# Kernel optimization log

Hardware: AMD Instinct MI355X
Metric: run time of the kernel (lower is better)

Reference implementation:

```python
import jax, jax.numpy as jnp
import numpy as np

BLOCK = 32          # per_1x32 microscaling block size along K
FP4_MAX = 6.0       # largest magnitude representable in e2m1
FP4_EMAX = 2.0      # exponent of largest fp4 binade (4..6)


def _quant_dequant_mxfp4(x):
    """Simulate MXFP4 (e2m1 elements, shared power-of-two E8M0 scale per 1x32
    block along the last dim): quantize then dequantize. x: [..., K], K % 32 == 0."""
    shape = x.shape
    xb = x.reshape(*shape[:-1], shape[-1] // BLOCK, BLOCK)
    amax = jnp.max(jnp.abs(xb), axis=-1, keepdims=True)
    # shared scale: 2^(floor(log2(amax)) - emax) so the block max lands in the top binade
    exp = jnp.floor(jnp.log2(jnp.maximum(amax, jnp.finfo(x.dtype).tiny))) - FP4_EMAX
    scale = jnp.where(amax > 0, jnp.exp2(exp), jnp.ones_like(amax))
    q = jnp.clip(xb / scale, -FP4_MAX, FP4_MAX)
    aq = jnp.abs(q)
    # e2m1 ulp: 0.5 on [0,2), 1 on [2,4), 2 on [4,6]
    lsb = jnp.where(aq < 2.0, 0.5, jnp.where(aq < 4.0, 1.0, 2.0))
    qr = jnp.round(q / lsb) * lsb  # round-to-nearest-even onto the fp4 grid
    return (qr * scale).reshape(shape)


def setup_inputs() -> dict:
    key = jax.random.key(0)
    k1, k2, k3 = jax.random.split(key, 3)
    B, S, K, N = 4, 2048, 2048, 2048
    inp = jax.random.normal(k1, (B, S, K), dtype=jnp.float32)
    weight = jax.random.normal(k2, (N, K), dtype=jnp.float32) * (1.0 / np.sqrt(K))
    bias = jax.random.normal(k3, (N,), dtype=jnp.float32) * 0.02
    return {"input": inp, "weight": weight, "bias": bias}


def reference(input, weight, bias):
    # both activation and weight are fake-quantized to MXFP4 per 1x32 blocks
    # along the contraction (in_features) dim, then a standard GEMM + bias.
    orig_shape = input.shape
    a = _quant_dequant_mxfp4(input.reshape(-1, orig_shape[-1]))  # [M, K]
    w = _quant_dequant_mxfp4(weight)                              # [N, K]
    out = jnp.einsum("mk,nk->mn", a, w) + bias
    return out.reshape(*orig_shape[:-1], weight.shape[0])
```

## Files before the change

kernel.cpp:

```cpp
#include <hip/hip_runtime.h>
#include <cstdint>


#define BM 128
#define BN 128
#define BK 128

typedef float floatx16 __attribute__((ext_vector_type(16)));
typedef int intx8 __attribute__((ext_vector_type(8)));

#define GLOBAL_AS __attribute__((address_space(1)))
#define LDS_AS __attribute__((address_space(3)))


__device__ __forceinline__ int enc1(float x, float inv) {
    float q = x * inv;
    q = fminf(fmaxf(q, -6.0f), 6.0f);
    int s = (int)(__float_as_uint(q) >> 31) << 3;
    float aq = fabsf(q);
    float ilsb = aq < 2.0f ? 2.0f : (aq < 4.0f ? 1.0f : 0.5f);
    float lsb  = aq < 2.0f ? 0.5f : (aq < 4.0f ? 1.0f : 2.0f);
    float ar = rintf(aq * ilsb) * lsb;
    int c;
    if (ar < 2.0f)      c = (int)(ar * 2.0f);
    else if (ar < 4.0f) c = 2 + (int)ar;
    else                c = 4 + (int)(ar * 0.5f);
    return c | s;
}

__global__ void quant_mxfp4_v4(const float* __restrict__ A, uint8_t* __restrict__ Aq,
                               uint8_t* __restrict__ AscT,
                               const float* __restrict__ W, uint8_t* __restrict__ Wq,
                               uint8_t* __restrict__ WscT,
                               long na4, long ntot4, int s4, long Mr, long Nr) {
    long t = (long)blockIdx.x * 256 + threadIdx.x;
    if (t >= ntot4) return;
    const float* src; uint8_t* dq; uint8_t* ds; long idx; long rows;
    if (t < na4) { src = A; dq = Aq; ds = AscT; idx = t; rows = Mr; }
    else         { src = W; dq = Wq; ds = WscT; idx = t - na4; rows = Nr; }

    float4 f = ((const float4*)src)[idx];
    float amax = fmaxf(fmaxf(fabsf(f.x), fabsf(f.y)),
                       fmaxf(fabsf(f.z), fabsf(f.w)));
    amax = fmaxf(amax, __shfl_xor(amax, 1));
    amax = fmaxf(amax, __shfl_xor(amax, 2));
    amax = fmaxf(amax, __shfl_xor(amax, 4));

    int ebits = (int)((__float_as_uint(amax) >> 23) & 0xff);
    int sb;
    float inv;
    if (amax > 0.0f) {
        sb = ebits - 2; if (sb < 0) sb = 0;
        inv = __uint_as_float((unsigned)((256 - ebits) & 255) << 23);
    } else {
        sb = 127;
        inv = 0.0f;
    }

    int c0 = enc1(f.x, inv), c1 = enc1(f.y, inv);
    int c2 = enc1(f.z, inv), c3 = enc1(f.w, inv);
    ((unsigned short*)dq)[idx] =
        (unsigned short)(c0 | (c1 << 4) | (c2 << 8) | (c3 << 12));
    if ((idx & 7) == 0) {
        long m  = idx >> s4;
        int  kb = (int)((idx & ((1L << s4) - 1)) >> 3);
        ds[(size_t)kb * rows + m] = (uint8_t)sb;
    }
}


__global__ __launch_bounds__(256, 4) void gemm_fp4_v6(
        const uint8_t* __restrict__ Aq, const uint8_t* __restrict__ AscT,
        const uint8_t* __restrict__ Wq, const uint8_t* __restrict__ WscT,
        const float* __restrict__ bias, float* __restrict__ C,
        int M, int N, int K) {
    __shared__ __align__(16) uint8_t sA[2][BM * 64];
    __shared__ __align__(16) uint8_t sB[2][BN * 64];

    const int tid = threadIdx.x;
    const int lane = tid & 63;
    const int w = tid >> 6;
    const int wr = w >> 1;
    const int wc = w & 1;
    const int row32 = lane & 31;
    const int q2 = lane >> 5;

    const int id = blockIdx.x;
    const int g = id & 7, h = id >> 3;
    const int by = g + 8 * (h & 7);
    const int bx = h >> 3;
    const int m0 = by * BM;
    const int n0 = bx * BN;
    const int KB2 = K >> 1;
    const int NT = K / BK;

    const int rA = wr * 64 + row32;
    const int rB = wc * 64 + row32;
    const int swz = (row32 >> 1) & 3;
    const int off0 = ((0 * 2 + q2) ^ swz) * 16;
    const int off1 = ((1 * 2 + q2) ^ swz) * 16;

    const uint8_t* pScA = AscT + (size_t)q2 * M + m0 + wr * 64 + row32;
    const uint8_t* pScB = WscT + (size_t)q2 * N + n0 + wc * 64 + row32;

    floatx16 acc[2][2];
#pragma unroll
    for (int i = 0; i < 2; i++)
#pragma unroll
        for (int j = 0; j < 2; j++)
#pragma unroll
            for (int r = 0; r < 16; r++) acc[i][j][r] = 0.f;

    auto stage = [&](int tt) {
        const int bb = tt & 1;
        const int kb = tt * 64;
#pragma unroll
        for (int it = 0; it < 2; ++it) {
            int idx = it * 256 + tid;
            int row = idx >> 2, c = idx & 3;
            int gc = c ^ ((row >> 1) & 3);
            const uint8_t* src = Aq + (size_t)(m0 + row) * KB2 + kb + gc * 16;
            __builtin_amdgcn_global_load_lds((GLOBAL_AS void*)src,
                (LDS_AS void*)(&sA[bb][idx * 16]), 16, 0, 0);
        }
#pragma unroll
        for (int it = 0; it < 2; ++it) {
            int idx = it * 256 + tid;
            int row = idx >> 2, c = idx & 3;
            int gc = c ^ ((row >> 1) & 3);
            const uint8_t* src = Wq + (size_t)(n0 + row) * KB2 + kb + gc * 16;
            __builtin_amdgcn_global_load_lds((GLOBAL_AS void*)src,
                (LDS_AS void*)(&sB[bb][idx * 16]), 16, 0, 0);
        }
    };

    stage(0);
    stage(1);
    asm volatile("s_waitcnt vmcnt(4)" ::: "memory");
    __builtin_amdgcn_sched_barrier(0);
    __builtin_amdgcn_s_barrier();

    for (int t = 0; t < NT; ++t) {
        const int p = t & 1;
        const uint8_t* pa = sA[p];
        const uint8_t* pb = sB[p];

        int sa[2][2], sb[2][2];
#pragma unroll
        for (int ks = 0; ks < 2; ++ks)
#pragma unroll
            for (int i = 0; i < 2; ++i) {
                sa[ks][i] = (int)pScA[(size_t)(2 * ks) * M + i * 32];
                sb[ks][i] = (int)pScB[(size_t)(2 * ks) * N + i * 32];
            }

        int4 fa[2][2], fb[2][2];
#pragma unroll
        for (int i = 0; i < 2; ++i) {
            fa[0][i] = *(const int4*)(pa + (rA + i * 32) * 64 + off0);
            fa[1][i] = *(const int4*)(pa + (rA + i * 32) * 64 + off1);
            fb[0][i] = *(const int4*)(pb + (rB + i * 32) * 64 + off0);
            fb[1][i] = *(const int4*)(pb + (rB + i * 32) * 64 + off1);
        }

        asm volatile("s_waitcnt lgkmcnt(0)" ::: "memory");
        __builtin_amdgcn_sched_barrier(0);
        __builtin_amdgcn_s_barrier();

        if (t + 2 < NT) stage(t + 2);

        if (t + 2 < NT) asm volatile("s_waitcnt vmcnt(4)" ::: "memory");
        else            asm volatile("s_waitcnt vmcnt(0)" ::: "memory");
        __builtin_amdgcn_sched_barrier(0);

        __builtin_amdgcn_s_setprio(1);
#pragma unroll
        for (int ks = 0; ks < 2; ++ks) {
            intx8 a0, a1, b0, b1;
            a0[0] = fa[ks][0].x; a0[1] = fa[ks][0].y; a0[2] = fa[ks][0].z; a0[3] = fa[ks][0].w;
            a1[0] = fa[ks][1].x; a1[1] = fa[ks][1].y; a1[2] = fa[ks][1].z; a1[3] = fa[ks][1].w;
            b0[0] = fb[ks][0].x; b0[1] = fb[ks][0].y; b0[2] = fb[ks][0].z; b0[3] = fb[ks][0].w;
            b1[0] = fb[ks][1].x; b1[1] = fb[ks][1].y; b1[2] = fb[ks][1].z; b1[3] = fb[ks][1].w;
#pragma unroll
            for (int z = 4; z < 8; ++z) { a0[z] = 0; a1[z] = 0; b0[z] = 0; b1[z] = 0; }
            acc[0][0] = __builtin_amdgcn_mfma_scale_f32_32x32x64_f8f6f4(
                a0, b0, acc[0][0], 4, 4, 0, sa[ks][0], 0, sb[ks][0]);
            acc[0][1] = __builtin_amdgcn_mfma_scale_f32_32x32x64_f8f6f4(
                a0, b1, acc[0][1], 4, 4, 0, sa[ks][0], 0, sb[ks][1]);
            acc[1][0] = __builtin_amdgcn_mfma_scale_f32_32x32x64_f8f6f4(
                a1, b0, acc[1][0], 4, 4, 0, sa[ks][1], 0, sb[ks][0]);
            acc[1][1] = __builtin_amdgcn_mfma_scale_f32_32x32x64_f8f6f4(
                a1, b1, acc[1][1], 4, 4, 0, sa[ks][1], 0, sb[ks][1]);
        }
        __builtin_amdgcn_s_setprio(0);
        __builtin_amdgcn_s_barrier();

        pScA += (size_t)4 * M;
        pScB += (size_t)4 * N;
    }

#pragma unroll
    for (int j = 0; j < 2; ++j) {
        int n = n0 + wc * 64 + j * 32 + row32;
        float bv = bias[n];
#pragma unroll
        for (int i = 0; i < 2; ++i) {
            int mb = m0 + wr * 64 + i * 32 + 4 * q2;
#pragma unroll
            for (int r = 0; r < 16; ++r) {
                int m = mb + (r & 3) + 8 * (r >> 2);
                C[(size_t)m * N + n] = acc[i][j][r] + bv;
            }
        }
    }
}


extern "C" void kernel_launch(void* const* d_in, const int* in_sizes, int n_in,
                              void* d_out, int out_size, void* d_ws, size_t ws_size,
                              hipStream_t stream) {
    const float* inp  = (const float*)d_in[0];
    const float* wgt  = (const float*)d_in[1];
    const float* bias = (const float*)d_in[2];
    float* out = (float*)d_out;

    const int N = in_sizes[2];
    const int K = in_sizes[1] / N;
    const long M = (long)in_sizes[0] / K;

    uint8_t* Aq4  = (uint8_t*)d_ws;
    uint8_t* Wq4  = Aq4 + (size_t)M * K / 2;
    uint8_t* AscT = Wq4 + (size_t)N * K / 2;
    uint8_t* WscT = AscT + (size_t)M * K / 32;

    int s4 = 0;
    while ((1 << s4) < (K >> 2)) ++s4;

    long na4   = (long)M * K / 4;
    long ntot4 = na4 + (long)N * K / 4;
    quant_mxfp4_v4<<<dim3((ntot4 + 255) / 256), dim3(256), 0, stream>>>(
        inp, Aq4, AscT, wgt, Wq4, WscT, na4, ntot4, s4, M, (long)N);

    dim3 grid((N / BN) * (int)(M / BM));
    gemm_fp4_v6<<<grid, dim3(256), 0, stream>>>(
        Aq4, AscT, Wq4, WscT, bias, out, (int)M, N, K);
}
```

Measured before the change: 153.1 us.

## Restructure GEMM pipeline: triple-buffer A, prefetch scales, one barrier per tile

```diff
diff --git a/kernel.cpp b/kernel.cpp
--- a/kernel.cpp
+++ b/kernel.cpp
@@ -69,13 +69,13 @@
 }
 
 
-__global__ __launch_bounds__(256, 4) void gemm_fp4_v6(
+__global__ __launch_bounds__(256, 4) void gemm_fp4_v7(
         const uint8_t* __restrict__ Aq, const uint8_t* __restrict__ AscT,
         const uint8_t* __restrict__ Wq, const uint8_t* __restrict__ WscT,
         const float* __restrict__ bias, float* __restrict__ C,
         int M, int N, int K) {
-    __shared__ __align__(16) uint8_t sA[2][BM * 64];
-    __shared__ __align__(16) uint8_t sB[2][BN * 64];
+    __shared__ __align__(16) uint8_t sAb[3][BM * 64];
+    __shared__ __align__(16) uint8_t sBb[2][BN * 64];
 
     const int tid = threadIdx.x;
     const int lane = tid & 63;
@@ -97,11 +97,8 @@
     const int rA = wr * 64 + row32;
     const int rB = wc * 64 + row32;
     const int swz = (row32 >> 1) & 3;
-    const int off0 = ((0 * 2 + q2) ^ swz) * 16;
-    const int off1 = ((1 * 2 + q2) ^ swz) * 16;
-
-    const uint8_t* pScA = AscT + (size_t)q2 * M + m0 + wr * 64 + row32;
-    const uint8_t* pScB = WscT + (size_t)q2 * N + n0 + wc * 64 + row32;
+    const int off0 = ((0 + q2) ^ swz) * 16;
+    const int off1 = ((2 + q2) ^ swz) * 16;
 
     floatx16 acc[2][2];
 #pragma unroll
@@ -111,8 +108,8 @@
 #pragma unroll
             for (int r = 0; r < 16; r++) acc[i][j][r] = 0.f;
 
-    auto stage = [&](int tt) {
-        const int bb = tt & 1;
+    auto stageA = [&](int tt) {
+        const int bb = tt % 3;
         const int kb = tt * 64;
 #pragma unroll
         for (int it = 0; it < 2; ++it) {
@@ -121,8 +118,12 @@
             int gc = c ^ ((row >> 1) & 3);
             const uint8_t* src = Aq + (size_t)(m0 + row) * KB2 + kb + gc * 16;
             __builtin_amdgcn_global_load_lds((GLOBAL_AS void*)src,
-                (LDS_AS void*)(&sA[bb][idx * 16]), 16, 0, 0);
-        }
+                (LDS_AS void*)(&sAb[bb][idx * 16]), 16, 0, 0);
+        }
+    };
+    auto stageB = [&](int tt) {
+        const int bb = tt & 1;
+        const int kb = tt * 64;
 #pragma unroll
         for (int it = 0; it < 2; ++it) {
             int idx = it * 256 + tid;
@@ -130,29 +131,27 @@
             int gc = c ^ ((row >> 1) & 3);
             const uint8_t* src = Wq + (size_t)(n0 + row) * KB2 + kb + gc * 16;
             __builtin_amdgcn_global_load_lds((GLOBAL_AS void*)src,
-                (LDS_AS void*)(&sB[bb][idx * 16]), 16, 0, 0);
-        }
-    };
-
-    stage(0);
-    stage(1);
-    asm volatile("s_waitcnt vmcnt(4)" ::: "memory");
-    __builtin_amdgcn_sched_barrier(0);
-    __builtin_amdgcn_s_barrier();
-
-    for (int t = 0; t < NT; ++t) {
-        const int p = t & 1;
-        const uint8_t* pa = sA[p];
-        const uint8_t* pb = sB[p];
-
-        int sa[2][2], sb[2][2];
+                (LDS_AS void*)(&sBb[bb][idx * 16]), 16, 0, 0);
+        }
+    };
+    auto loadScales = [&](int tt, int (&sa)[2][2], int (&sb)[2][2]) {
 #pragma unroll
         for (int ks = 0; ks < 2; ++ks)
 #pragma unroll
             for (int i = 0; i < 2; ++i) {
-                sa[ks][i] = (int)pScA[(size_t)(2 * ks) * M + i * 32];
-                sb[ks][i] = (int)pScB[(size_t)(2 * ks) * N + i * 32];
+                sa[ks][i] = (int)AscT[(size_t)(4 * tt + 2 * ks + q2) * M +
+                                      m0 + wr * 64 + i * 32 + row32];
+                sb[ks][i] = (int)WscT[(size_t)(4 * tt + 2 * ks + q2) * N +
+                                      n0 + wc * 64 + i * 32 + row32];
             }
+    };
+
+    intx8 a0 = {0,0,0,0,0,0,0,0}, a1 = a0, b0 = a0, b1 = a0;
+
+    auto tile = [&](int t, int (&saU)[2][2], int (&sbU)[2][2],
+                    int (&saL)[2][2], int (&sbL)[2][2]) {
+        const uint8_t* pa = sAb[t % 3];
+        const uint8_t* pb = sBb[t & 1];
 
         int4 fa[2][2], fb[2][2];
 #pragma unroll
@@ -163,40 +162,59 @@
             fb[1][i] = *(const int4*)(pb + (rB + i * 32) * 64 + off1);
         }
 
+        if (t + 1 < NT) loadScales(t + 1, saL, sbL);
+        __builtin_amdgcn_sched_barrier(0);
+        if (t + 1 < NT) stageB(t + 1);
+        __builtin_amdgcn_sched_barrier(0);
+        if (t + 2 < NT) stageA(t + 2);
+        __builtin_amdgcn_sched_barrier(0);
+
         asm volatile("s_waitcnt lgkmcnt(0)" ::: "memory");
         __builtin_amdgcn_sched_barrier(0);
-        __builtin_amdgcn_s_barrier();
-
-        if (t + 2 < NT) stage(t + 2);
-
-        if (t + 2 < NT) asm volatile("s_waitcnt vmcnt(4)" ::: "memory");
-        else            asm volatile("s_waitcnt vmcnt(0)" ::: "memory");
-        __builtin_amdgcn_sched_barrier(0);
 
         __builtin_amdgcn_s_setprio(1);
 #pragma unroll
         for (int ks = 0; ks < 2; ++ks) {
-            intx8 a0, a1, b0, b1;
-            a0[0] = fa[ks][0].x; a0[1] = fa[ks][0].y; a0[2] = fa[ks][0].z; a0[3] = fa[ks][0].w;
-            a1[0] = fa[ks][1].x; a1[1] = fa[ks][1].y; a1[2] = fa[ks][1].z; a1[3] = fa[ks][1].w;
-            b0[0] = fb[ks][0].x; b0[1] = fb[ks][0].y; b0[2] = fb[ks][0].z; b0[3] = fb[ks][0].w;
-            b1[0] = fb[ks][1].x; b1[1] = fb[ks][1].y; b1[2] = fb[ks][1].z; b1[3] = fb[ks][1].w;
-#pragma unroll
-            for (int z = 4; z < 8; ++z) { a0[z] = 0; a1[z] = 0; b0[z] = 0; b1[z] = 0; }
+            const int4 fA0 = fa[ks][0], fA1 = fa[ks][1];
+            const int4 fB0 = fb[ks][0], fB1 = fb[ks][1];
+            a0[0] = fA0.x; a0[1] = fA0.y; a0[2] = fA0.z; a0[3] = fA0.w;
+            a1[0] = fA1.x; a1[1] = fA1.y; a1[2] = fA1.z; a1[3] = fA1.w;
+            b0[0] = fB0.x; b0[1] = fB0.y; b0[2] = fB0.z; b0[3] = fB0.w;
+            b1[0] = fB1.x; b1[1] = fB1.y; b1[2] = fB1.z; b1[3] = fB1.w;
             acc[0][0] = __builtin_amdgcn_mfma_scale_f32_32x32x64_f8f6f4(
-                a0, b0, acc[0][0], 4, 4, 0, sa[ks][0], 0, sb[ks][0]);
+                a0, b0, acc[0][0], 4, 4, 0, saU[ks][0], 0, sbU[ks][0]);
             acc[0][1] = __builtin_amdgcn_mfma_scale_f32_32x32x64_f8f6f4(
-                a0, b1, acc[0][1], 4, 4, 0, sa[ks][0], 0, sb[ks][1]);
+                a0, b1, acc[0][1], 4, 4, 0, saU[ks][0], 0, sbU[ks][1]);
             acc[1][0] = __builtin_amdgcn_mfma_scale_f32_32x32x64_f8f6f4(
-                a1, b0, acc[1][0], 4, 4, 0, sa[ks][1], 0, sb[ks][0]);
+                a1, b0, acc[1][0], 4, 4, 0, saU[ks][1], 0, sbU[ks][0]);
             acc[1][1] = __builtin_amdgcn_mfma_scale_f32_32x32x64_f8f6f4(
-                a1, b1, acc[1][1], 4, 4, 0, sa[ks][1], 0, sb[ks][1]);
+                a1, b1, acc[1][1], 4, 4, 0, saU[ks][1], 0, sbU[ks][1]);
         }
         __builtin_amdgcn_s_setprio(0);
-        __builtin_amdgcn_s_barrier();
-
-        pScA += (size_t)4 * M;
-        pScB += (size_t)4 * N;
+
+        if (t + 2 < NT)      asm volatile("s_waitcnt vmcnt(2)" ::: "memory");
+        else if (t + 1 < NT) asm volatile("s_waitcnt vmcnt(0)" ::: "memory");
+        __builtin_amdgcn_sched_barrier(0);
+        if (t + 1 < NT) __builtin_amdgcn_s_barrier();
+    };
+
+    int sa0[2][2], sb0[2][2], sa1[2][2], sb1[2][2];
+
+    stageA(0);
+    __builtin_amdgcn_sched_barrier(0);
+    stageB(0);
+    __builtin_amdgcn_sched_barrier(0);
+    loadScales(0, sa0, sb0);
+    __builtin_amdgcn_sched_barrier(0);
+    stageA(1);
+    __builtin_amdgcn_sched_barrier(0);
+    asm volatile("s_waitcnt vmcnt(2)" ::: "memory");
+    __builtin_amdgcn_sched_barrier(0);
+    __builtin_amdgcn_s_barrier();
+
+    for (int t = 0; t < NT; t += 2) {
+        tile(t,     sa0, sb0, sa1, sb1);
+        tile(t + 1, sa1, sb1, sa0, sb0);
     }
 
 #pragma unroll
@@ -242,6 +260,6 @@
         inp, Aq4, AscT, wgt, Wq4, WscT, na4, ntot4, s4, M, (long)N);
 
     dim3 grid((N / BN) * (int)(M / BM));
-    gemm_fp4_v6<<<grid, dim3(256), 0, stream>>>(
+    gemm_fp4_v7<<<grid, dim3(256), 0, stream>>>(
         Aq4, AscT, Wq4, WscT, bias, out, (int)M, N, K);
 }
```

New measurement: 418.6 us. +173.5%, slower.
